# Kernel tuning notes

Measured on AMD Instinct MI355X. Metric: run time of the kernel, lower is better.

## Reference

```python
import jax, jax.numpy as jnp
import numpy as np

B, LQ, LK, DK, DV = 16, 1024, 1024, 256, 256
NEG = -1e9


def setup_inputs() -> dict:
    key = jax.random.key(0)
    kq, kk, kv, kw, km = jax.random.split(key, 5)
    return {
        "query": jax.random.normal(kq, (B, LQ, DK), dtype=jnp.float32),
        "key": jax.random.normal(kk, (B, LK, DK), dtype=jnp.float32),
        "value": jax.random.normal(kv, (B, LK, DV), dtype=jnp.float32),
        "w": jax.random.normal(kw, (DK,), dtype=jnp.float32),  # Linear(d_k,1,bias=False) weight
        "mask": jax.random.randint(km, (B, LQ, LK), 0, 2, dtype=jnp.int32),
    }


def reference(query, key, value, w, mask):
    # Bahdanau additive score: alignment_layer(query[:, :, None] + key[:, None, :]).squeeze(-1)
    # Exact linear decomposition: W·(q+k) = W·q + W·k, avoiding the (Lq,Lk,d_k) intermediate.
    q_s = jnp.einsum("bqd,d->bq", query, w)  # [B, Lq]
    k_s = jnp.einsum("bkd,d->bk", key, w)    # [B, Lk]
    scores = q_s[:, :, None] + k_s[:, None, :]  # [B, Lq, Lk]
    scores = jnp.where(mask == 0, NEG, scores)
    p_attn = jax.nn.softmax(scores, axis=-1)
    return jnp.matmul(p_attn, value)  # [B, Lq, Dv]
```

## Files before the change

### kernel.cpp

```cpp
#include <hip/hip_runtime.h>
#include <math.h>


#define NB     16
#define NL     1024
#define ND     256
#define NSTAGE 56
#define NBKT   128

__global__ __launch_bounds__(256)
void ks_kernel(const float* __restrict__ key, const float* __restrict__ w,
               float* __restrict__ ks) {
    int wid  = threadIdx.x >> 6;
    int lane = threadIdx.x & 63;
    int row  = blockIdx.x * 4 + wid;
    const float4* krow = (const float4*)(key + (size_t)row * ND);
    float4 kv = krow[lane];
    float4 wv = ((const float4*)w)[lane];
    float p = kv.x * wv.x + kv.y * wv.y + kv.z * wv.z + kv.w * wv.w;
    #pragma unroll
    for (int off = 32; off > 0; off >>= 1)
        p += __shfl_xor(p, off, 64);
    if (lane == 0) ks[row] = p;
}

__global__ __launch_bounds__(1024)
void select_kernel(const float* __restrict__ ks,
                   float* __restrict__ e_s, int* __restrict__ idx_s,
                   float* __restrict__ rem) {
    __shared__ float red[NL];
    __shared__ float se[NL];
    __shared__ int   cnt[NBKT];
    __shared__ int   cur[NBKT];
    __shared__ float csum[16];
    const int b = blockIdx.x;
    const int t = threadIdx.x;
    const int lane = t & 63;
    const int wid  = t >> 6;

    float v = ks[b * NL + t];

    red[t] = v;
    __syncthreads();
    for (int off = 512; off > 0; off >>= 1) {
        if (t < off) red[t] = fmaxf(red[t], red[t + off]);
        __syncthreads();
    }
    const float m = red[0];
    __syncthreads();

    const float e = __expf(v - m);

    if (t < NBKT) cnt[t] = 0;
    __syncthreads();
    int bkt = (int)fminf(m - v, (float)(NBKT - 1));
    atomicAdd(&cnt[bkt], 1);
    __syncthreads();

    if (t < NBKT) cur[t] = cnt[t];
    __syncthreads();
    for (int off = 1; off < NBKT; off <<= 1) {
        int add = 0;
        if (t < NBKT && t >= off) add = cur[t - off];
        __syncthreads();
        if (t < NBKT) cur[t] += add;
        __syncthreads();
    }
    if (t < NBKT) cur[t] -= cnt[t];
    __syncthreads();

    int p = atomicAdd(&cur[bkt], 1);
    se[p] = e;
    e_s  [b * NL + p] = e;
    idx_s[b * NL + p] = t;
    __syncthreads();

    float s = se[wid * 64 + lane];
    #pragma unroll
    for (int off = 32; off > 0; off >>= 1)
        s += __shfl_xor(s, off, 64);
    if (lane == 0) csum[wid] = s;
    __syncthreads();

    if (t == 0) {
        float run = 0.0f;
        for (int c = 15; c >= 0; --c) {
            rem[b * NL + c * 64 + 63] = run;
            run += csum[c];
        }
    }
}

__global__ __launch_bounds__(1024)
void attn_kernel(const float* __restrict__ value, const int* __restrict__ mask,
                 const float* __restrict__ e_s, const int* __restrict__ idx_s,
                 const float* __restrict__ rem, float* __restrict__ out) {
    __shared__ float          lds_V[NSTAGE * ND];
    __shared__ unsigned short mbits[16][64];
    __shared__ float          lds_e[64];
    __shared__ int            lds_idx[64];

    const int wid  = threadIdx.x >> 6;
    const int lane = threadIdx.x & 63;
    const int row  = blockIdx.x * 16 + wid;
    const int b    = row >> 10;
    const int base = b << 10;

    if (threadIdx.x < 64) {
        lds_e[threadIdx.x]   = e_s[base + threadIdx.x];
        lds_idx[threadIdx.x] = idx_s[base + threadIdx.x];
    }
    __syncthreads();

    const float4* vbase = (const float4*)(value + ((size_t)b << 10) * ND);

    for (int r = wid; r < NSTAGE; r += 16)
        ((float4*)lds_V)[r * 64 + lane] = vbase[(size_t)lds_idx[r] * 64 + lane];

    const int4* mrow4 = (const int4*)(mask + (size_t)row * NL);
    unsigned int bits = 0;
    #pragma unroll
    for (int j = 0; j < 4; ++j) {
        int4 m = mrow4[lane * 4 + j];
        bits |= (m.x != 0 ? 1u : 0u) << (j * 4 + 0);
        bits |= (m.y != 0 ? 1u : 0u) << (j * 4 + 1);
        bits |= (m.z != 0 ? 1u : 0u) << (j * 4 + 2);
        bits |= (m.w != 0 ? 1u : 0u) << (j * 4 + 3);
    }
    mbits[wid][lane] = (unsigned short)bits;
    __syncthreads();

    float4 acc = make_float4(0.f, 0.f, 0.f, 0.f);
    float Z = 0.0f;

    #pragma unroll 8
    for (int i = 0; i < 64; ++i) {
        int k = lds_idx[i];
        if ((mbits[wid][k >> 4] >> (k & 15)) & 1) {
            float ei = lds_e[i];
            Z += ei;
            float4 v;
            if (i < NSTAGE) v = ((const float4*)lds_V)[i * 64 + lane];
            else            v = vbase[(size_t)k * 64 + lane];
            acc.x += ei * v.x; acc.y += ei * v.y;
            acc.z += ei * v.z; acc.w += ei * v.w;
        }
    }
    bool done = (rem[base + 63] <= 1e-5f * Z);

    for (int c = 1; c < 16 && !done; ++c) {
        const int o = base + c * 64;
        float e_r = e_s[o + lane];
        int   k_r = idx_s[o + lane];
        #pragma unroll 8
        for (int i = 0; i < 64; ++i) {
            int k = __shfl(k_r, i);
            if ((mbits[wid][k >> 4] >> (k & 15)) & 1) {
                float ei = __shfl(e_r, i);
                Z += ei;
                float4 v = vbase[(size_t)k * 64 + lane];
                acc.x += ei * v.x; acc.y += ei * v.y;
                acc.z += ei * v.z; acc.w += ei * v.w;
            }
        }
        done = (rem[o + 63] <= 1e-5f * Z);
    }

    float4* orow = (float4*)(out + (size_t)row * ND);
    if (Z > 0.0f) {
        float inv = 1.0f / Z;
        orow[lane] = make_float4(acc.x * inv, acc.y * inv, acc.z * inv, acc.w * inv);
    } else {
        float4 s = make_float4(0.f, 0.f, 0.f, 0.f);
        for (int k = 0; k < NL; ++k) {
            float4 v = vbase[(size_t)k * 64 + lane];
            s.x += v.x; s.y += v.y; s.z += v.z; s.w += v.w;
        }
        const float inv = 1.0f / (float)NL;
        orow[lane] = make_float4(s.x * inv, s.y * inv, s.z * inv, s.w * inv);
    }
}

extern "C" void kernel_launch(void* const* d_in, const int* in_sizes, int n_in,
                              void* d_out, int out_size, void* d_ws, size_t ws_size,
                              hipStream_t stream) {
    const float* key   = (const float*)d_in[1];
    const float* value = (const float*)d_in[2];
    const float* w     = (const float*)d_in[3];
    const int*   mask  = (const int*)d_in[4];
    float*       outp  = (float*)d_out;

    float* ks    = (float*)d_ws;
    float* e_s   = ks + NB * NL;
    int*   idx_s = (int*)(e_s + NB * NL);
    float* rem   = (float*)(idx_s + NB * NL);

    ks_kernel    <<<NB * NL / 4, 256, 0, stream>>>(key, w, ks);
    select_kernel<<<NB, 1024, 0, stream>>>(ks, e_s, idx_s, rem);
    attn_kernel  <<<NB * NL / 16, 1024, 0, stream>>>(value, mask, e_s, idx_s, rem, outp);
}
```

Baseline: 189.3 us.

## Read mask entries on demand and drop LDS staging in attention kernel

Measured after the change: 322.1 us. +70.1%, slower.

```diff
diff --git a/kernel.cpp b/kernel.cpp
--- a/kernel.cpp
+++ b/kernel.cpp
@@ -5,7 +5,6 @@
 #define NB     16
 #define NL     1024
 #define ND     256
-#define NSTAGE 56
 #define NBKT   128
 
 __global__ __launch_bounds__(256)
@@ -26,8 +25,7 @@
 
 __global__ __launch_bounds__(1024)
 void select_kernel(const float* __restrict__ ks,
-                   float* __restrict__ e_s, int* __restrict__ idx_s,
-                   float* __restrict__ rem) {
+                   float2* __restrict__ pk, float* __restrict__ rem) {
     __shared__ float red[NL];
     __shared__ float se[NL];
     __shared__ int   cnt[NBKT];
@@ -71,8 +69,7 @@
 
     int p = atomicAdd(&cur[bkt], 1);
     se[p] = e;
-    e_s  [b * NL + p] = e;
-    idx_s[b * NL + p] = t;
+    pk[b * NL + p] = make_float2(e, __int_as_float(t));
     __syncthreads();
 
     float s = se[wid * 64 + lane];
@@ -91,79 +88,39 @@
     }
 }
 
-__global__ __launch_bounds__(1024)
+__global__ __launch_bounds__(256)
 void attn_kernel(const float* __restrict__ value, const int* __restrict__ mask,
-                 const float* __restrict__ e_s, const int* __restrict__ idx_s,
-                 const float* __restrict__ rem, float* __restrict__ out) {
-    __shared__ float          lds_V[NSTAGE * ND];
-    __shared__ unsigned short mbits[16][64];
-    __shared__ float          lds_e[64];
-    __shared__ int            lds_idx[64];
-
+                 const float2* __restrict__ pk, const float* __restrict__ rem,
+                 float* __restrict__ out) {
     const int wid  = threadIdx.x >> 6;
     const int lane = threadIdx.x & 63;
-    const int row  = blockIdx.x * 16 + wid;
+    const int row  = blockIdx.x * 4 + wid;
     const int b    = row >> 10;
     const int base = b << 10;
 
-    if (threadIdx.x < 64) {
-        lds_e[threadIdx.x]   = e_s[base + threadIdx.x];
-        lds_idx[threadIdx.x] = idx_s[base + threadIdx.x];
-    }
-    __syncthreads();
-
-    const float4* vbase = (const float4*)(value + ((size_t)b << 10) * ND);
-
-    for (int r = wid; r < NSTAGE; r += 16)
-        ((float4*)lds_V)[r * 64 + lane] = vbase[(size_t)lds_idx[r] * 64 + lane];
-
-    const int4* mrow4 = (const int4*)(mask + (size_t)row * NL);
-    unsigned int bits = 0;
-    #pragma unroll
-    for (int j = 0; j < 4; ++j) {
-        int4 m = mrow4[lane * 4 + j];
-        bits |= (m.x != 0 ? 1u : 0u) << (j * 4 + 0);
-        bits |= (m.y != 0 ? 1u : 0u) << (j * 4 + 1);
-        bits |= (m.z != 0 ? 1u : 0u) << (j * 4 + 2);
-        bits |= (m.w != 0 ? 1u : 0u) << (j * 4 + 3);
-    }
-    mbits[wid][lane] = (unsigned short)bits;
-    __syncthreads();
+    const float4*  vbase = (const float4*)(value + ((size_t)b << 10) * ND);
+    const int*     mrow  = mask + (size_t)row * NL;
+    const float2*  pk_g  = pk + base;
 
     float4 acc = make_float4(0.f, 0.f, 0.f, 0.f);
     float Z = 0.0f;
+    bool done = false;
 
-    #pragma unroll 8
-    for (int i = 0; i < 64; ++i) {
-        int k = lds_idx[i];
-        if ((mbits[wid][k >> 4] >> (k & 15)) & 1) {
-            float ei = lds_e[i];
-            Z += ei;
-            float4 v;
-            if (i < NSTAGE) v = ((const float4*)lds_V)[i * 64 + lane];
-            else            v = vbase[(size_t)k * 64 + lane];
-            acc.x += ei * v.x; acc.y += ei * v.y;
-            acc.z += ei * v.z; acc.w += ei * v.w;
-        }
-    }
-    bool done = (rem[base + 63] <= 1e-5f * Z);
-
-    for (int c = 1; c < 16 && !done; ++c) {
-        const int o = base + c * 64;
-        float e_r = e_s[o + lane];
-        int   k_r = idx_s[o + lane];
+    for (int c = 0; c < 16 && !done; ++c) {
+        const int o = c * 64;
         #pragma unroll 8
         for (int i = 0; i < 64; ++i) {
-            int k = __shfl(k_r, i);
-            if ((mbits[wid][k >> 4] >> (k & 15)) & 1) {
-                float ei = __shfl(e_r, i);
+            float2 p = pk_g[o + i];
+            int   k  = __float_as_int(p.y);
+            if (mrow[k] != 0) {
+                float ei = p.x;
                 Z += ei;
                 float4 v = vbase[(size_t)k * 64 + lane];
                 acc.x += ei * v.x; acc.y += ei * v.y;
                 acc.z += ei * v.z; acc.w += ei * v.w;
             }
         }
-        done = (rem[o + 63] <= 1e-5f * Z);
+        done = (rem[base + o + 63] <= 1e-5f * Z);
     }
 
     float4* orow = (float4*)(out + (size_t)row * ND);
@@ -190,12 +147,11 @@
     const int*   mask  = (const int*)d_in[4];
     float*       outp  = (float*)d_out;
 
-    float* ks    = (float*)d_ws;
-    float* e_s   = ks + NB * NL;
-    int*   idx_s = (int*)(e_s + NB * NL);
-    float* rem   = (float*)(idx_s + NB * NL);
+    float*  ks  = (float*)d_ws;
+    float2* pkb = (float2*)(ks + NB * NL);
+    float*  rem = (float*)(pkb + NB * NL);
 
     ks_kernel    <<<NB * NL / 4, 256, 0, stream>>>(key, w, ks);
-    select_kernel<<<NB, 1024, 0, stream>>>(ks, e_s, idx_s, rem);
-    attn_kernel  <<<NB * NL / 16, 1024, 0, stream>>>(value, mask, e_s, idx_s, rem, outp);
+    select_kernel<<<NB, 1024, 0, stream>>>(ks, pkb, rem);
+    attn_kernel  <<<NB * NL / 4, 256, 0, stream>>>(value, mask, pkb, rem, outp);
 }
```
